# Optimization experiments

Measured on AMD Instinct MI355X. Metric: run time of the kernel, lower is better.

The kernel has to match this reference:

```python
import jax, jax.numpy as jnp
import numpy as np

APP_DIM = 27
FEA_PE = 6
VIEW_PE = 6
FEATURE_C = 128
DENSITY_SHIFT = -10.0
DISTANCE_SCALE = 25.0
IN_MLPC = 2 * VIEW_PE * 3 + 2 * FEA_PE * APP_DIM + 3 + APP_DIM  # 390


def positional_encoding(x, freqs):
    # x: [..., C] -> [..., 2*freqs*C]
    freq_bands = (2.0 ** jnp.arange(freqs)).astype(x.dtype)
    pts = (x[..., None] * freq_bands).reshape(x.shape[:-1] + (freqs * x.shape[-1],))
    return jnp.concatenate([jnp.sin(pts), jnp.cos(pts)], axis=-1)


def alpha2weights(alpha):
    # alpha: [N_rays, N_samples]; last sample forced opaque (as in source)
    alpha = alpha.at[:, -1].set(1.0)
    trans = jnp.concatenate(
        [jnp.ones((alpha.shape[0], 1), alpha.dtype), 1.0 - alpha + 1e-10], axis=-1)
    T = jnp.cumprod(trans, axis=-1)
    weights = alpha * T[:, :-1]
    return weights, T


def setup_inputs() -> dict:
    key = jax.random.key(0)
    ks = jax.random.split(key, 12)
    N_rays, N_samples = 4096, 128
    sigma_feat = jax.random.normal(ks[0], (N_rays, N_samples), jnp.float32)
    app_features = 0.1 * jax.random.normal(ks[1], (N_rays, N_samples, APP_DIM), jnp.float32)
    vd = jax.random.normal(ks[2], (N_rays, N_samples, 3), jnp.float32)
    viewdirs = vd / (jnp.linalg.norm(vd, axis=-1, keepdims=True) + 1e-8)
    dists = 0.02 * jax.random.uniform(ks[3], (N_rays, N_samples), jnp.float32)

    def linear(k, fan_in, fan_out):
        kw, kb = jax.random.split(k)
        lim = 1.0 / np.sqrt(fan_in)
        W = jax.random.uniform(kw, (fan_in, fan_out), jnp.float32, -lim, lim)
        b = jax.random.uniform(kb, (fan_out,), jnp.float32, -lim, lim)
        return W, b

    W1, b1 = linear(ks[4], IN_MLPC, FEATURE_C)
    W2, b2 = linear(ks[5], FEATURE_C, FEATURE_C)
    W3, _ = linear(ks[6], FEATURE_C, 3)
    b3 = jnp.zeros((3,), jnp.float32)  # bias of last layer initialized to 0 in source
    return {"sigma_feat": sigma_feat, "app_features": app_features,
            "viewdirs": viewdirs, "dists": dists,
            "W1": W1, "b1": b1, "W2": W2, "b2": b2, "W3": W3, "b3": b3}


def reference(sigma_feat, app_features, viewdirs, dists, W1, b1, W2, b2, W3, b3):
    # feature2density: softplus with density_shift
    sigma = jax.nn.softplus(sigma_feat + DENSITY_SHIFT)
    alpha = 1.0 - jnp.exp(-sigma * dists * DISTANCE_SCALE)  # [N_rays, N_samples]
    weights, _T = alpha2weights(alpha)

    # MLPRender_Fea: cat[features, viewdirs, PE(features), PE(viewdirs)]
    mlp_in = jnp.concatenate(
        [app_features, viewdirs,
         positional_encoding(app_features, FEA_PE),
         positional_encoding(viewdirs, VIEW_PE)], axis=-1)  # [R, S, 390]
    h = jax.nn.relu(jnp.einsum('rsc,cf->rsf', mlp_in, W1) + b1)
    h = jax.nn.relu(jnp.einsum('rsf,fg->rsg', h, W2) + b2)
    rgb = jax.nn.sigmoid(jnp.einsum('rsg,go->rso', h, W3) + b3)  # [R, S, 3]

    rgb_map = jnp.sum(weights[..., None] * rgb, axis=-2)  # [R, 3]
    return rgb_map
```

## Files before the change

### kernel.cpp

```cpp
#include <hip/hip_runtime.h>
#include <math.h>

typedef unsigned short u16;
using bf16x8 = __attribute__((ext_vector_type(8))) short;
using f32x4  = __attribute__((ext_vector_type(4))) float;

#define NS      128
#define NBLOCKS 4096
#define NSLICE  17

#define POOLSZ 32768

#define BAR() do { asm volatile("s_waitcnt lgkmcnt(0)" ::: "memory");        \
                   __builtin_amdgcn_s_barrier();                              \
                   asm volatile("" ::: "memory"); } while (0)

#define MF(A,B,C) __builtin_amdgcn_mfma_f32_16x16x32_bf16((A),(B),(C),0,0,0)

__device__ __forceinline__ u16 f2bf(float f) {
    unsigned int i = __float_as_uint(f);
    return (u16)((i + 0x7FFFu + ((i >> 16) & 1u)) >> 16);
}

__device__ __forceinline__ unsigned pk(float hi, float lo) {
    unsigned r;
    asm("v_cvt_pk_bf16_f32 %0, %1, %2" : "=v"(r) : "v"(lo), "v"(hi));
    return r;
}
__device__ __forceinline__ u16 f2bf1(float f) {
    return (u16)((__float_as_uint(f) + 0x8000u) >> 16);
}

__device__ __forceinline__ int afoff_h1(int m, int k) {
    int e = (k >> 3) & 3;
    int chunk = (m >> 4) * 64 + e * 16 + (m & 15);
    return ((5 + (k >> 5)) & 7) * 4096 + (chunk ^ e) * 8 + (k & 7);
}
__device__ __forceinline__ int afoff_h2(int m, int k) {
    int e = (k >> 3) & 3;
    int chunk = (m >> 4) * 64 + e * 16 + (m & 15);
    return ((1 + (k >> 5)) & 7) * 4096 + (chunk ^ e) * 8 + (k & 7);
}

__device__ __forceinline__ int orig_k(int ch, int slot) {
    if (ch < 27) {
        if (slot == 0) return ch;
        if (slot <= 6) return 30 + ch * 6 + (slot - 1);
        return 192 + ch * 6 + (slot - 7);
    } else {
        int c = ch - 27;
        if (slot == 0) return 27 + c;
        if (slot <= 6) return 354 + c * 6 + (slot - 1);
        return 372 + c * 6 + (slot - 7);
    }
}

__device__ __forceinline__ int cons_slot(int j) {
    if (j == 0) return 0;
    return (j & 1) ? (j + 1) / 2 : 6 + j / 2;
}

__global__ __launch_bounds__(256) void prep_kernel(
    const float* __restrict__ W1, const float* __restrict__ W2,
    const float* __restrict__ W3, u16* __restrict__ ws)
{
    int idx = blockIdx.x * 256 + threadIdx.x;
    if (idx < 53248) {
        int jj = idx & 7, lane = (idx >> 3) & 63, nt = (idx >> 9) & 7, j = idx >> 12;
        int q = lane >> 4, l15 = lane & 15;
        int ch = q * 8 + jj;
        int n = nt * 16 + l15;
        ws[idx] = (ch < 30) ? f2bf(W1[orig_k(ch, cons_slot(j)) * 128 + n]) : (u16)0;
    } else if (idx < 69632) {
        int i2 = idx - 53248;
        int jj = i2 & 7, lane = (i2 >> 3) & 63, nt = (i2 >> 9) & 7, ks = i2 >> 12;
        int k = ks * 32 + (lane >> 4) * 8 + jj;
        int n = nt * 16 + (lane & 15);
        ws[idx] = f2bf(W2[k * 128 + n]);
    } else if (idx < 71680) {
        int i3 = idx - 69632;
        int jj = i3 & 7, lane = (i3 >> 3) & 63, ks = i3 >> 9;
        int k = ks * 32 + (lane >> 4) * 8 + jj;
        int n = lane & 15;
        ws[idx] = (n < 3) ? f2bf(W3[k * 3 + n]) : (u16)0;
    }
}

#define LOADB2(N0, N1, s)                                                     \
    if ((s) < NSLICE) {                                                       \
        const u16* wp = wp0 + (s) * 4096;                                     \
        N0 = *(const bf16x8*)(wp);                                            \
        N1 = *(const bf16x8*)(wp + 512);                                      \
    }

#define BODYX(s, C0,C1, N0,N1)                                                \
  {                                                                           \
    LOADB2(N0, N1, (s)+2);                                                    \
    const u16* ab = pool + ((s)&7)*4096 + (wm*256 + lane)*8;                  \
    bf16x8 a0 = *(const bf16x8*)(ab);                                         \
    bf16x8 a1 = *(const bf16x8*)(ab + 512);                                   \
    __builtin_amdgcn_s_setprio(1);                                            \
    acc[0][0]=MF(a0,C0,acc[0][0]); acc[0][1]=MF(a0,C1,acc[0][1]);             \
    acc[1][0]=MF(a1,C0,acc[1][0]); acc[1][1]=MF(a1,C1,acc[1][1]);             \
    a0 = *(const bf16x8*)(ab + 1024);                                         \
    a1 = *(const bf16x8*)(ab + 1536);                                         \
    acc[2][0]=MF(a0,C0,acc[2][0]); acc[2][1]=MF(a0,C1,acc[2][1]);             \
    acc[3][0]=MF(a1,C0,acc[3][0]); acc[3][1]=MF(a1,C1,acc[3][1]);             \
    __builtin_amdgcn_s_setprio(0);                                            \
  }

#define BODYH(s, C0,C1, N0,N1)                                                \
  {                                                                           \
    LOADB2(N0, N1, (s)+2);                                                    \
    int cb = ((5 + ((s)-13)) & 7) * 512 + ((wm*256 + lane) ^ quad);           \
    bf16x8 a0 = *(const bf16x8*)(pool + cb*8);                                \
    bf16x8 a1 = *(const bf16x8*)(pool + (cb+64)*8);                           \
    __builtin_amdgcn_s_setprio(1);                                            \
    acc[0][0]=MF(a0,C0,acc[0][0]); acc[0][1]=MF(a0,C1,acc[0][1]);             \
    acc[1][0]=MF(a1,C0,acc[1][0]); acc[1][1]=MF(a1,C1,acc[1][1]);             \
    a0 = *(const bf16x8*)(pool + (cb+128)*8);                                 \
    a1 = *(const bf16x8*)(pool + (cb+192)*8);                                 \
    acc[2][0]=MF(a0,C0,acc[2][0]); acc[2][1]=MF(a0,C1,acc[2][1]);             \
    acc[3][0]=MF(a1,C0,acc[3][0]); acc[3][1]=MF(a1,C1,acc[3][1]);             \
    __builtin_amdgcn_s_setprio(0);                                            \
  }

#define W8(j, A)                                                              \
  { uint4 w_; w_.x = pk(A[1],A[0]); w_.y = pk(A[3],A[2]);                     \
    w_.z = pk(A[5],A[4]); w_.w = pk(A[7],A[6]);                               \
    *(uint4*)(pool + ((j)&7)*4096 + bx2) = w_; }

#define DBL(d)                                                                \
  { _Pragma("unroll")                                                         \
    for (int i_ = 0; i_ < 8; ++i_) {                                          \
        float t_ = sreg[i_] * creg[i_];                                       \
        float u_ = creg[i_] * creg[i_] - sreg[i_] * sreg[i_];                 \
        sreg[i_] = t_ + t_; creg[i_] = u_;                                    \
    }                                                                         \
    W8(1 + 2*(d), sreg); W8(2 + 2*(d), creg); }

__global__ __launch_bounds__(512, 4) void render_kernel(
    const float* __restrict__ sigma_g, const float* __restrict__ app_g,
    const float* __restrict__ view_g,  const float* __restrict__ dists_g,
    const float* __restrict__ b1_g,    const float* __restrict__ b2_g,
    const float* __restrict__ b3_g,    const u16* __restrict__ ws,
    float* __restrict__ out_g)
{
    __shared__ __align__(16) u16 pool[POOLSZ];
    __shared__ __align__(16) float part[NS * 3];
    __shared__ float scanS;
    __shared__ float sum2[6];

    const int tid  = threadIdx.x;
    const int lane = tid & 63;
    const int wave = tid >> 6;
    const int l15  = lane & 15;
    const int quad = lane >> 4;
    const int wm   = wave >> 2;
    const int wn   = wave & 3;

    const int r  = blockIdx.x;
    const int rb = r * NS;
    const int row = tid & 127;
    const int g   = tid >> 7;
    const float* ap = app_g  + (rb + row) * 27;
    const float* vp = view_g + (rb + row) * 3;
    const int bx2 = ((row >> 4) * 64 + g * 16 + (row & 15)) * 8;

    const u16* wp0 = ws + (wn * 128 + lane) * 8;
    bf16x8 bP0, bP1, bQ0, bQ1, bR0, bR1;
    LOADB2(bP0, bP1, 0);
    LOADB2(bQ0, bQ1, 1);

    float v8[8];
    #pragma unroll
    for (int i = 0; i < 8; ++i) {
        int ch = g * 8 + i;
        v8[i] = (ch < 27) ? ap[ch] : ((ch < 30) ? vp[ch - 27] : 0.f);
    }

    float alpha = 0.f, prod = 1.f, wr = 0.f;
    if (tid < NS) {
        float x  = sigma_g[rb + tid] - 10.f;
        float sp = (x > 20.f) ? x : log1pf(expf(x));
        alpha = 1.f - expf(-sp * dists_g[rb + tid] * 25.f);
        if (tid == NS - 1) alpha = 1.f;
        float tb = 1.f - alpha + 1e-10f;
        prod = tb;
        #pragma unroll
        for (int d = 1; d < 64; d <<= 1) {
            float v = __shfl_up(prod, d);
            if (lane >= d) prod *= v;
        }
        if (tid == 63) scanS = prod;
    }

    float sreg[8], creg[8];
    #pragma unroll
    for (int i = 0; i < 8; ++i) {
        float rev = v8[i] * 0.15915494309189535f;
        rev -= floorf(rev);
        sreg[i] = __builtin_amdgcn_sinf(rev);
        creg[i] = __builtin_amdgcn_cosf(rev);
    }
    W8(0, v8); W8(1, sreg); W8(2, creg);
    BAR();

    if (tid < NS) {
        float prev = __shfl_up(prod, 1);
        float base = (lane == 0) ? 1.f : prev;
        float scale = (wave == 1) ? scanS : 1.f;
        wr = alpha * base * scale;
    }

    const f32x4 vzero = {0.f, 0.f, 0.f, 0.f};
    f32x4 acc[4][2];
    #pragma unroll
    for (int mt = 0; mt < 4; ++mt)
        #pragma unroll
        for (int nt = 0; nt < 2; ++nt) acc[mt][nt] = vzero;

    BODYX(0,  bP0,bP1, bR0,bR1);
    BODYX(1,  bQ0,bQ1, bP0,bP1);
    BODYX(2,  bR0,bR1, bQ0,bQ1);
    DBL(1); DBL(2);
    BAR();
    BODYX(3,  bP0,bP1, bR0,bR1);
    BODYX(4,  bQ0,bQ1, bP0,bP1);
    BODYX(5,  bR0,bR1, bQ0,bQ1);
    BODYX(6,  bP0,bP1, bR0,bR1);
    DBL(3); DBL(4);
    BAR();
    BODYX(7,  bQ0,bQ1, bP0,bP1);
    BODYX(8,  bR0,bR1, bQ0,bQ1);
    BODYX(9,  bP0,bP1, bR0,bR1);
    BODYX(10, bQ0,bQ1, bP0,bP1);
    DBL(5);
    BAR();
    BODYX(11, bR0,bR1, bQ0,bQ1);
    const float b1r0 = b1_g[wn * 32 + l15];
    const float b1r1 = b1_g[wn * 32 + 16 + l15];
    BODYX(12, bP0,bP1, bR0,bR1);

    #pragma unroll
    for (int mt = 0; mt < 4; ++mt)
        #pragma unroll
        for (int nt = 0; nt < 2; ++nt) {
            int col = wn * 32 + nt * 16 + l15;
            #pragma unroll
            for (int rr = 0; rr < 4; ++rr) {
                int rw = wm * 64 + mt * 16 + quad * 4 + rr;
                pool[afoff_h1(rw, col)] =
                    f2bf1(fmaxf(acc[mt][nt][rr] + ((nt == 0) ? b1r0 : b1r1), 0.f));
            }
            acc[mt][nt] = vzero;
        }
    BAR();

    const float b2r0 = b2_g[wn * 32 + l15];
    const float b2r1 = b2_g[wn * 32 + 16 + l15];

    BODYH(13, bQ0,bQ1, bP0,bP1);
    BODYH(14, bR0,bR1, bQ0,bQ1);
    BODYH(15, bP0,bP1, bR0,bR1);
    BODYH(16, bQ0,bQ1, bP0,bP1);

    #pragma unroll
    for (int mt = 0; mt < 4; ++mt)
        #pragma unroll
        for (int nt = 0; nt < 2; ++nt) {
            int col = wn * 32 + nt * 16 + l15;
            #pragma unroll
            for (int rr = 0; rr < 4; ++rr) {
                int rw = wm * 64 + mt * 16 + quad * 4 + rr;
                pool[afoff_h2(rw, col)] =
                    f2bf1(fmaxf(acc[mt][nt][rr] + ((nt == 0) ? b2r0 : b2r1), 0.f));
            }
        }
    BAR();

    const u16* w3r = ws + 69632;
    const float b3v = (l15 < 3) ? b3_g[l15] : 0.f;
    f32x4 acc3 = vzero;
    #pragma unroll
    for (int ks = 0; ks < 4; ++ks) {
        bf16x8 w3f = *(const bf16x8*)(w3r + (ks * 64 + lane) * 8);
        int c = ((1 + ks) & 7) * 512 + ((wave * 64 + lane) ^ quad);
        bf16x8 a3 = *(const bf16x8*)(pool + c * 8);
        acc3 = MF(a3, w3f, acc3);
    }
    if (l15 < 3) {
        #pragma unroll
        for (int rr = 0; rr < 4; ++rr) {
            int rw = wave * 16 + quad * 4 + rr;
            float v = acc3[rr] + b3v;
            part[rw * 3 + l15] = 1.f / (1.f + expf(-v));
        }
    }
    BAR();

    if (tid < NS) {
        float v0 = wr * part[tid * 3 + 0];
        float v1 = wr * part[tid * 3 + 1];
        float v2 = wr * part[tid * 3 + 2];
        #pragma unroll
        for (int d = 1; d < 64; d <<= 1) {
            v0 += __shfl_xor(v0, d);
            v1 += __shfl_xor(v1, d);
            v2 += __shfl_xor(v2, d);
        }
        if (lane == 0) {
            sum2[wave * 3 + 0] = v0;
            sum2[wave * 3 + 1] = v1;
            sum2[wave * 3 + 2] = v2;
        }
    }
    BAR();
    if (tid == 0) {
        out_g[r * 3 + 0] = sum2[0] + sum2[3];
        out_g[r * 3 + 1] = sum2[1] + sum2[4];
        out_g[r * 3 + 2] = sum2[2] + sum2[5];
    }
}

extern "C" void kernel_launch(void* const* d_in, const int* in_sizes, int n_in,
                              void* d_out, int out_size, void* d_ws, size_t ws_size,
                              hipStream_t stream) {
    (void)in_sizes; (void)n_in; (void)out_size; (void)ws_size;
    const float* sigma = (const float*)d_in[0];
    const float* app   = (const float*)d_in[1];
    const float* view  = (const float*)d_in[2];
    const float* dists = (const float*)d_in[3];
    const float* W1    = (const float*)d_in[4];
    const float* b1    = (const float*)d_in[5];
    const float* W2    = (const float*)d_in[6];
    const float* b2    = (const float*)d_in[7];
    const float* W3    = (const float*)d_in[8];
    const float* b3    = (const float*)d_in[9];
    float* out = (float*)d_out;

    u16* ws = (u16*)d_ws;

    prep_kernel<<<280, 256, 0, stream>>>(W1, W2, W3, ws);
    render_kernel<<<NBLOCKS, 512, 0, stream>>>(sigma, app, view, dists,
                                               b1, b2, b3, ws, out);
}
```

Before: 195.1 us.

## Shrink LDS pool to six slices and raise occupancy to six blocks

The shared-memory ring shrinks from 8 to 6 slices of 4096 bf16 (64KB to 48KB). Launch bounds rise from 4 to 6 blocks per CU, and weight prefetch depth drops from two slices ahead to one, removing a register triple-buffer. The PE doubling writes are spread across more barriers so slices can be reused, and the hidden layers are written into slots 0-3 behind extra barriers. More resident blocks should hide latency better, at the cost of shallower prefetch, more barriers, and a tighter register budget that may spill.

Measured after the change: 280.0 us. 43.5% more time.

```diff
diff --git a/kernel.cpp b/kernel.cpp
--- a/kernel.cpp
+++ b/kernel.cpp
@@ -9,7 +9,7 @@
 #define NBLOCKS 4096
 #define NSLICE  17
 
-#define POOLSZ 32768
+#define POOLSZ 24576
 
 #define BAR() do { asm volatile("s_waitcnt lgkmcnt(0)" ::: "memory");        \
                    __builtin_amdgcn_s_barrier();                              \
@@ -31,15 +31,10 @@
     return (u16)((__float_as_uint(f) + 0x8000u) >> 16);
 }
 
-__device__ __forceinline__ int afoff_h1(int m, int k) {
+__device__ __forceinline__ int afoff_h(int m, int k) {
     int e = (k >> 3) & 3;
     int chunk = (m >> 4) * 64 + e * 16 + (m & 15);
-    return ((5 + (k >> 5)) & 7) * 4096 + (chunk ^ e) * 8 + (k & 7);
-}
-__device__ __forceinline__ int afoff_h2(int m, int k) {
-    int e = (k >> 3) & 3;
-    int chunk = (m >> 4) * 64 + e * 16 + (m & 15);
-    return ((1 + (k >> 5)) & 7) * 4096 + (chunk ^ e) * 8 + (k & 7);
+    return (k >> 5) * 4096 + (chunk ^ e) * 8 + (k & 7);
 }
 
 __device__ __forceinline__ int orig_k(int ch, int slot) {
@@ -95,8 +90,8 @@
 
 #define BODYX(s, C0,C1, N0,N1)                                                \
   {                                                                           \
-    LOADB2(N0, N1, (s)+2);                                                    \
-    const u16* ab = pool + ((s)&7)*4096 + (wm*256 + lane)*8;                  \
+    LOADB2(N0, N1, (s)+1);                                                    \
+    const u16* ab = pool + ((s)%6)*4096 + (wm*256 + lane)*8;                  \
     bf16x8 a0 = *(const bf16x8*)(ab);                                         \
     bf16x8 a1 = *(const bf16x8*)(ab + 512);                                   \
     __builtin_amdgcn_s_setprio(1);                                            \
@@ -111,8 +106,8 @@
 
 #define BODYH(s, C0,C1, N0,N1)                                                \
   {                                                                           \
-    LOADB2(N0, N1, (s)+2);                                                    \
-    int cb = ((5 + ((s)-13)) & 7) * 512 + ((wm*256 + lane) ^ quad);           \
+    LOADB2(N0, N1, (s)+1);                                                    \
+    int cb = ((s)-13) * 512 + ((wm*256 + lane) ^ quad);                       \
     bf16x8 a0 = *(const bf16x8*)(pool + cb*8);                                \
     bf16x8 a1 = *(const bf16x8*)(pool + (cb+64)*8);                           \
     __builtin_amdgcn_s_setprio(1);                                            \
@@ -128,7 +123,7 @@
 #define W8(j, A)                                                              \
   { uint4 w_; w_.x = pk(A[1],A[0]); w_.y = pk(A[3],A[2]);                     \
     w_.z = pk(A[5],A[4]); w_.w = pk(A[7],A[6]);                               \
-    *(uint4*)(pool + ((j)&7)*4096 + bx2) = w_; }
+    *(uint4*)(pool + ((j)%6)*4096 + bx2) = w_; }
 
 #define DBL(d)                                                                \
   { _Pragma("unroll")                                                         \
@@ -139,7 +134,7 @@
     }                                                                         \
     W8(1 + 2*(d), sreg); W8(2 + 2*(d), creg); }
 
-__global__ __launch_bounds__(512, 4) void render_kernel(
+__global__ __launch_bounds__(512, 6) void render_kernel(
     const float* __restrict__ sigma_g, const float* __restrict__ app_g,
     const float* __restrict__ view_g,  const float* __restrict__ dists_g,
     const float* __restrict__ b1_g,    const float* __restrict__ b2_g,
@@ -168,9 +163,8 @@
     const int bx2 = ((row >> 4) * 64 + g * 16 + (row & 15)) * 8;
 
     const u16* wp0 = ws + (wn * 128 + lane) * 8;
-    bf16x8 bP0, bP1, bQ0, bQ1, bR0, bR1;
+    bf16x8 bP0, bP1, bQ0, bQ1;
     LOADB2(bP0, bP1, 0);
-    LOADB2(bQ0, bQ1, 1);
 
     float v8[8];
     #pragma unroll
@@ -220,27 +214,27 @@
         #pragma unroll
         for (int nt = 0; nt < 2; ++nt) acc[mt][nt] = vzero;
 
-    BODYX(0,  bP0,bP1, bR0,bR1);
+    BODYX(0,  bP0,bP1, bQ0,bQ1);
     BODYX(1,  bQ0,bQ1, bP0,bP1);
-    BODYX(2,  bR0,bR1, bQ0,bQ1);
-    DBL(1); DBL(2);
-    BAR();
-    BODYX(3,  bP0,bP1, bR0,bR1);
-    BODYX(4,  bQ0,bQ1, bP0,bP1);
-    BODYX(5,  bR0,bR1, bQ0,bQ1);
-    BODYX(6,  bP0,bP1, bR0,bR1);
-    DBL(3); DBL(4);
-    BAR();
+    DBL(1);  BAR();
+    BODYX(2,  bP0,bP1, bQ0,bQ1);
+    BODYX(3,  bQ0,bQ1, bP0,bP1);
+    DBL(2);  BAR();
+    BODYX(4,  bP0,bP1, bQ0,bQ1);
+    BODYX(5,  bQ0,bQ1, bP0,bP1);
+    DBL(3);  BAR();
+    BODYX(6,  bP0,bP1, bQ0,bQ1);
     BODYX(7,  bQ0,bQ1, bP0,bP1);
-    BODYX(8,  bR0,bR1, bQ0,bQ1);
-    BODYX(9,  bP0,bP1, bR0,bR1);
-    BODYX(10, bQ0,bQ1, bP0,bP1);
-    DBL(5);
-    BAR();
-    BODYX(11, bR0,bR1, bQ0,bQ1);
+    DBL(4);  BAR();
+    BODYX(8,  bP0,bP1, bQ0,bQ1);
+    BODYX(9,  bQ0,bQ1, bP0,bP1);
+    DBL(5);  BAR();
+    BODYX(10, bP0,bP1, bQ0,bQ1);
+    BODYX(11, bQ0,bQ1, bP0,bP1);
     const float b1r0 = b1_g[wn * 32 + l15];
     const float b1r1 = b1_g[wn * 32 + 16 + l15];
-    BODYX(12, bP0,bP1, bR0,bR1);
+    BODYX(12, bP0,bP1, bQ0,bQ1);
+    BAR();
 
     #pragma unroll
     for (int mt = 0; mt < 4; ++mt)
@@ -250,7 +244,7 @@
             #pragma unroll
             for (int rr = 0; rr < 4; ++rr) {
                 int rw = wm * 64 + mt * 16 + quad * 4 + rr;
-                pool[afoff_h1(rw, col)] =
+                pool[afoff_h(rw, col)] =
                     f2bf1(fmaxf(acc[mt][nt][rr] + ((nt == 0) ? b1r0 : b1r1), 0.f));
             }
             acc[mt][nt] = vzero;
@@ -261,9 +255,10 @@
     const float b2r1 = b2_g[wn * 32 + 16 + l15];
 
     BODYH(13, bQ0,bQ1, bP0,bP1);
-    BODYH(14, bR0,bR1, bQ0,bQ1);
-    BODYH(15, bP0,bP1, bR0,bR1);
-    BODYH(16, bQ0,bQ1, bP0,bP1);
+    BODYH(14, bP0,bP1, bQ0,bQ1);
+    BODYH(15, bQ0,bQ1, bP0,bP1);
+    BODYH(16, bP0,bP1, bQ0,bQ1);
+    BAR();
 
     #pragma unroll
     for (int mt = 0; mt < 4; ++mt)
@@ -273,7 +268,7 @@
             #pragma unroll
             for (int rr = 0; rr < 4; ++rr) {
                 int rw = wm * 64 + mt * 16 + quad * 4 + rr;
-                pool[afoff_h2(rw, col)] =
+                pool[afoff_h(rw, col)] =
                     f2bf1(fmaxf(acc[mt][nt][rr] + ((nt == 0) ? b2r0 : b2r1), 0.f));
             }
         }
@@ -285,7 +280,7 @@
     #pragma unroll
     for (int ks = 0; ks < 4; ++ks) {
         bf16x8 w3f = *(const bf16x8*)(w3r + (ks * 64 + lane) * 8);
-        int c = ((1 + ks) & 7) * 512 + ((wave * 64 + lane) ^ quad);
+        int c = ks * 512 + ((wave * 64 + lane) ^ quad);
         bf16x8 a3 = *(const bf16x8*)(pool + c * 8);
         acc3 = MF(a3, w3f, acc3);
     }
```
